# Performance work log

Hardware: AMD Instinct MI355X
Metric: run time of the kernel (lower is better)

The kernel has to match this reference:

```python
import jax, jax.numpy as jnp
import numpy as np

INPUT, HIDDEN, OUTPUT = 512, 1024, 512


def setup_inputs() -> dict:
    key = jax.random.key(0)
    k1, k2, k3, k4, k5 = jax.random.split(key, 5)
    fan = INPUT + HIDDEN
    s = 1.0 / np.sqrt(fan)
    so = 1.0 / np.sqrt(HIDDEN)
    return {
        "x": jax.random.normal(k1, (64, 512, INPUT), dtype=jnp.float32),
        "W": jax.random.uniform(k2, (fan, 4 * HIDDEN), jnp.float32, -s, s),
        "b": jax.random.uniform(k3, (4 * HIDDEN,), jnp.float32, -s, s),
        "W_out": jax.random.uniform(k4, (HIDDEN, OUTPUT), jnp.float32, -so, so),
        "b_out": jax.random.uniform(k5, (OUTPUT,), jnp.float32, -so, so),
    }


def reference(x, W, b, W_out, b_out):
    B, T, _ = x.shape
    h = HIDDEN
    h0 = jnp.zeros((B, h), dtype=x.dtype)
    c0 = jnp.zeros((B, h), dtype=x.dtype)

    def step(carry, xt):
        hs, cs = carry
        # fused gate pre-activation: [B, 4h]
        f = jnp.concatenate([xt, hs], axis=1) @ W + b
        fg = jax.nn.sigmoid(f[:, :h])          # forget gate
        ig = jax.nn.sigmoid(f[:, h:2 * h])     # input gate
        gg = jnp.tanh(f[:, 2 * h:3 * h])       # candidate
        og = jax.nn.sigmoid(f[:, 3 * h:])      # output gate
        cs = cs * fg + ig * gg
        hs = og * jnp.tanh(cs)
        return (hs, cs), None

    (hT, _), _ = jax.lax.scan(step, (h0, c0), jnp.swapaxes(x, 0, 1))
    return hT @ W_out + b_out
```

## Files before the change

### kernel.cpp

```cpp
#include <hip/hip_runtime.h>


#define B_   64
#define T_   512
#define IN_  512
#define H_   1024
#define G4_  4096
#define OUT_ 512

typedef _Float16 f16;
typedef _Float16 f16x8 __attribute__((ext_vector_type(8)));
typedef _Float16 f16x4 __attribute__((ext_vector_type(4)));
typedef float f32x4  __attribute__((ext_vector_type(4)));
typedef float f32x16 __attribute__((ext_vector_type(16)));

#define X16_OFF   0UL
#define WOT_OFF   33554432UL
#define H_OFF     (WOT_OFF + 1048576UL)
#define FLG_OFF   (H_OFF + 262144UL)
#define WS_NEED   (FLG_OFF + 8192UL)
#define ZERO_BYTES (262144UL + 8192UL)

__device__ __forceinline__ float sigmoidf_(float v) { return 1.f / (1.f + __expf(-v)); }
__device__ __forceinline__ float tanhf_(float v) { return 1.f - 2.f / (__expf(2.f * v) + 1.f); }

__device__ __forceinline__ f16x8 ld_agent_b128(const f16* p) {
  f16x8 r;
  asm volatile("global_load_dwordx4 %0, %1, off sc0 sc1" : "=v"(r) : "v"(p));
  return r;
}

__device__ __forceinline__ void st_agent_b128(f16* p, f16x8 v) {
  asm volatile("global_store_dwordx4 %0, %1, off sc0 sc1" :: "v"(p), "v"(v) : "memory");
}

__device__ __forceinline__ void wait_vm0() {
  asm volatile("s_waitcnt vmcnt(0)" ::: "memory");
  __builtin_amdgcn_sched_barrier(0);
}

__global__ __launch_bounds__(256) void lstm_prepass(
    const float* __restrict__ x, const float* __restrict__ Wout,
    f16* __restrict__ x16, f16* __restrict__ WoT) {
  long i = (long)blockIdx.x * blockDim.x + threadIdx.x;
  long stride = (long)gridDim.x * blockDim.x;
  const long n4 = (long)B_ * T_ * IN_ / 4;
  const float4* x4 = (const float4*)x;
  f16x4* o4 = (f16x4*)x16;
  for (long p = i; p < n4; p += stride) {
    float4 v = x4[p];
    f16x4 o = { (f16)v.x, (f16)v.y, (f16)v.z, (f16)v.w };
    o4[p] = o;
  }
  const long nw = (long)H_ * OUT_;
  for (long p = i; p < nw; p += stride) {
    long k = p / OUT_, c = p % OUT_;
    WoT[c * (long)H_ + k] = (f16)Wout[p];
  }
}

__global__ __launch_bounds__(512, 2) void lstm_main(
    const float* __restrict__ W, const float* __restrict__ b,
    const f16* __restrict__ x16, f16* hbuf, unsigned int* flags) {

  const int wg   = blockIdx.x;
  const int g    = wg >> 6;
  const int wgi  = wg & 63;
  const int tid  = threadIdx.x;
  const int wave = tid >> 6;
  const int lane = tid & 63;

  const int hbase   = wgi * 16;
  const int colLane = lane & 31;
  const int khalf   = (lane >> 5) * 8;
  const int arow    = lane & 31;

  f16x8 wf[24];
  #pragma unroll
  for (int n = 0; n < 2; ++n) {
    const int gate = n * 2 + (colLane >> 4);
    const int gcol = gate * H_ + hbase + (colLane & 15);
    #pragma unroll
    for (int kf = 0; kf < 12; ++kf) {
      const int k0 = (kf < 4) ? (64 * wave + 16 * kf)
                              : (512 + 128 * wave + 16 * (kf - 4));
      f16x8 v;
      #pragma unroll
      for (int j = 0; j < 8; ++j)
        v[j] = (f16)W[(long)(k0 + khalf + j) * G4_ + gcol];
      wf[n * 12 + kf] = v;
    }
  }

  const int erow = tid >> 4;
  const int ej   = tid & 15;
  float bias[4];
  #pragma unroll
  for (int gt = 0; gt < 4; ++gt) bias[gt] = b[gt * H_ + hbase + ej];

  float c_state = 0.f;

  __shared__ float red[8][32][68];
  __shared__ f16 hshare[32][16];

  const f16* xg   = x16 + (long)(g * 32) * T_ * IN_;
  f16* hb         = hbuf + (long)g * 2 * 32 * H_;
  unsigned int* flg = flags + g * 64 * 16;

  f32x16 acc0 = {}, acc1 = {};
  {
    const f16* xrow = xg + (long)arow * (T_ * IN_) + 64 * wave + khalf;
    f16x8 xa[4];
    #pragma unroll
    for (int f = 0; f < 4; ++f) xa[f] = *(const f16x8*)(xrow + 16 * f);
    #pragma unroll
    for (int kf = 0; kf < 4; ++kf) {
      acc0 = __builtin_amdgcn_mfma_f32_32x32x16_f16(xa[kf], wf[kf],      acc0, 0, 0, 0);
      acc1 = __builtin_amdgcn_mfma_f32_32x32x16_f16(xa[kf], wf[12 + kf], acc1, 0, 0, 0);
    }
  }

  for (int t = 0; t < T_; ++t) {
    if (t > 0) {
      const unsigned int tgt = (unsigned int)t;
      const unsigned int* fp = &flg[(8 * wave + (lane & 7)) << 4];
      long guard = 0;
      for (;;) {
        unsigned int v = __hip_atomic_load(fp, __ATOMIC_RELAXED,
                                           __HIP_MEMORY_SCOPE_AGENT);
        if (__all(v >= tgt) || ++guard > (1L << 22)) break;
      }
    }

    {
      const f16* hrow = hb + (long)(t & 1) * (32 * H_) + (long)arow * H_
                           + 128 * wave + khalf;
      f16x8 ha[8];
      #pragma unroll
      for (int f = 0; f < 8; ++f)
        ha[f] = ld_agent_b128(hrow + 16 * f);
      wait_vm0();
      #pragma unroll
      for (int kf = 0; kf < 8; ++kf) {
        acc0 = __builtin_amdgcn_mfma_f32_32x32x16_f16(ha[kf], wf[4 + kf],  acc0, 0, 0, 0);
        acc1 = __builtin_amdgcn_mfma_f32_32x32x16_f16(ha[kf], wf[16 + kf], acc1, 0, 0, 0);
      }
    }

    #pragma unroll
    for (int r = 0; r < 16; ++r) {
      const int row = (r & 3) + 8 * (r >> 2) + 4 * (lane >> 5);
      red[wave][row][colLane]      = acc0[r];
      red[wave][row][32 + colLane] = acc1[r];
    }
    __syncthreads();

    float f4[4];
    #pragma unroll
    for (int gt = 0; gt < 4; ++gt) {
      float s = bias[gt];
      #pragma unroll
      for (int w = 0; w < 8; ++w) s += red[w][erow][gt * 16 + ej];
      f4[gt] = s;
    }
    const float fg = sigmoidf_(f4[0]);
    const float ig = sigmoidf_(f4[1]);
    const float gg = tanhf_(f4[2]);
    const float og = sigmoidf_(f4[3]);
    c_state = c_state * fg + ig * gg;
    hshare[erow][ej] = (f16)(og * tanhf_(c_state));
    __syncthreads();

    if (wave == 0) {
      const int row = lane >> 1, half = lane & 1;
      f16x8 hv = *(const f16x8*)&hshare[row][half * 8];
      st_agent_b128(&hb[(long)((t + 1) & 1) * (32 * H_) + (long)row * H_
                        + hbase + half * 8], hv);
      wait_vm0();
      if (lane == 0)
        __hip_atomic_store(&flg[wgi << 4], (unsigned int)(t + 1),
                           __ATOMIC_RELAXED, __HIP_MEMORY_SCOPE_AGENT);
    }

    acc0 = f32x16{}; acc1 = f32x16{};
    if (t + 1 < T_) {
      const f16* xrow = xg + (long)arow * (T_ * IN_) + (long)(t + 1) * IN_
                           + 64 * wave + khalf;
      f16x8 xa[4];
      #pragma unroll
      for (int f = 0; f < 4; ++f) xa[f] = *(const f16x8*)(xrow + 16 * f);
      #pragma unroll
      for (int kf = 0; kf < 4; ++kf) {
        acc0 = __builtin_amdgcn_mfma_f32_32x32x16_f16(xa[kf], wf[kf],      acc0, 0, 0, 0);
        acc1 = __builtin_amdgcn_mfma_f32_32x32x16_f16(xa[kf], wf[12 + kf], acc1, 0, 0, 0);
      }
    }
  }
}

__global__ __launch_bounds__(256) void lstm_out(
    const f16* __restrict__ hbuf, const f16* __restrict__ WoT,
    const float* __restrict__ bout, float* __restrict__ out) {
  const int wgid = blockIdx.x;
  const int rowT = wgid >> 5;
  const int colT = wgid & 31;
  const int tid  = threadIdx.x;
  const int wave = tid >> 6;
  const int lane = tid & 63;
  const int r16  = lane & 15;
  const int ksel = (lane >> 4) * 8;

  const int g = rowT >> 1;
  const f16* hrow = hbuf + (long)g * 2 * 32 * H_
                  + (long)((rowT & 1) * 16 + r16) * H_;
  const f16* wrow = WoT + (long)(colT * 16 + r16) * H_;

  f32x4 acc = {};
  #pragma unroll
  for (int f = 0; f < 8; ++f) {
    f16x8 a  = *(const f16x8*)(hrow + 256 * wave + 32 * f + ksel);
    f16x8 bf = *(const f16x8*)(wrow + 256 * wave + 32 * f + ksel);
    acc = __builtin_amdgcn_mfma_f32_16x16x32_f16(a, bf, acc, 0, 0, 0);
  }

  __shared__ float red[4][16][20];
  #pragma unroll
  for (int r = 0; r < 4; ++r)
    red[wave][(lane >> 4) * 4 + r][lane & 15] = acc[r];
  __syncthreads();

  const int row = tid >> 4;
  const int col = tid & 15;
  float s = bout[colT * 16 + col];
  #pragma unroll
  for (int w = 0; w < 4; ++w) s += red[w][row][col];
  out[(long)(rowT * 16 + row) * OUT_ + colT * 16 + col] = s;
}

extern "C" void kernel_launch(void* const* d_in, const int* in_sizes, int n_in,
                              void* d_out, int out_size, void* d_ws, size_t ws_size,
                              hipStream_t stream) {
  const float* x    = (const float*)d_in[0];
  const float* W    = (const float*)d_in[1];
  const float* b    = (const float*)d_in[2];
  const float* Wout = (const float*)d_in[3];
  const float* bout = (const float*)d_in[4];
  float* out = (float*)d_out;

  if (ws_size < WS_NEED) return;

  char* wsb = (char*)d_ws;
  f16* x16  = (f16*)(wsb + X16_OFF);
  f16* WoT  = (f16*)(wsb + WOT_OFF);
  f16* hbuf = (f16*)(wsb + H_OFF);
  unsigned int* flags = (unsigned int*)(wsb + FLG_OFF);

  hipMemsetAsync(wsb + H_OFF, 0, ZERO_BYTES, stream);

  lstm_prepass<<<1024, 256, 0, stream>>>(x, Wout, x16, WoT);

  lstm_main<<<128, 512, 0, stream>>>(W, b, x16, hbuf, flags);

  lstm_out<<<128, 256, 0, stream>>>(hbuf, WoT, bout, out);
}
```

Measured before the change: 2.450 ms.

## Replace per-step flags with step tags encoded in the hidden-state values

Removes the separate flag array. Each hidden value is stored in fp32 as the step tag (t mod 4) plus 0.4*h. Readers poll the h buffer directly until every 8-value chunk is within 0.5 of the expected tag, then decode it to fp16. This drops the store → wait → flag-store → flag-poll → load chain, the LDS staging of h and one __syncthreads per step; the reduction buffer is also double-buffered. In exchange the h traffic doubles, since it is fp32 with per-thread scalar stores, and correctness relies on |h| < 1 and on each 16-byte load being observed as a unit.

```diff
diff --git a/kernel.cpp b/kernel.cpp
--- a/kernel.cpp
+++ b/kernel.cpp
@@ -17,25 +17,30 @@
 #define X16_OFF   0UL
 #define WOT_OFF   33554432UL
 #define H_OFF     (WOT_OFF + 1048576UL)
-#define FLG_OFF   (H_OFF + 262144UL)
-#define WS_NEED   (FLG_OFF + 8192UL)
-#define ZERO_BYTES (262144UL + 8192UL)
+#define WS_NEED   (H_OFF + 524288UL)
+#define ZERO_BYTES 524288UL
+
+#define ENCK 0.4f
+#define DECK 2.5f
 
 __device__ __forceinline__ float sigmoidf_(float v) { return 1.f / (1.f + __expf(-v)); }
 __device__ __forceinline__ float tanhf_(float v) { return 1.f - 2.f / (__expf(2.f * v) + 1.f); }
 
-__device__ __forceinline__ f16x8 ld_agent_b128(const f16* p) {
-  f16x8 r;
+__device__ __forceinline__ f32x4 ld_agent_f32x4(const float* p) {
+  f32x4 r;
   asm volatile("global_load_dwordx4 %0, %1, off sc0 sc1" : "=v"(r) : "v"(p));
   return r;
 }
-
-__device__ __forceinline__ void st_agent_b128(f16* p, f16x8 v) {
-  asm volatile("global_store_dwordx4 %0, %1, off sc0 sc1" :: "v"(p), "v"(v) : "memory");
+__device__ __forceinline__ void st_agent_f32(float* p, float v) {
+  asm volatile("global_store_dword %0, %1, off sc0 sc1" :: "v"(p), "v"(v) : "memory");
 }
 
 __device__ __forceinline__ void wait_vm0() {
   asm volatile("s_waitcnt vmcnt(0)" ::: "memory");
+  __builtin_amdgcn_sched_barrier(0);
+}
+__device__ __forceinline__ void wait_vm1() {
+  asm volatile("s_waitcnt vmcnt(1)" ::: "memory");
   __builtin_amdgcn_sched_barrier(0);
 }
 
@@ -61,7 +66,7 @@
 
 __global__ __launch_bounds__(512, 2) void lstm_main(
     const float* __restrict__ W, const float* __restrict__ b,
-    const f16* __restrict__ x16, f16* hbuf, unsigned int* flags) {
+    const f16* __restrict__ x16, float* hbuf) {
 
   const int wg   = blockIdx.x;
   const int g    = wg >> 6;
@@ -100,12 +105,10 @@
 
   float c_state = 0.f;
 
-  __shared__ float red[8][32][68];
-  __shared__ f16 hshare[32][16];
-
-  const f16* xg   = x16 + (long)(g * 32) * T_ * IN_;
-  f16* hb         = hbuf + (long)g * 2 * 32 * H_;
-  unsigned int* flg = flags + g * 64 * 16;
+  __shared__ float red[2][8][32][68];
+
+  const f16* xg = x16 + (long)(g * 32) * T_ * IN_;
+  float* hb     = hbuf + (long)g * 2 * 32 * H_;
 
   f32x16 acc0 = {}, acc1 = {};
   {
@@ -121,74 +124,95 @@
   }
 
   for (int t = 0; t < T_; ++t) {
-    if (t > 0) {
-      const unsigned int tgt = (unsigned int)t;
-      const unsigned int* fp = &flg[(8 * wave + (lane & 7)) << 4];
-      long guard = 0;
-      for (;;) {
-        unsigned int v = __hip_atomic_load(fp, __ATOMIC_RELAXED,
-                                           __HIP_MEMORY_SCOPE_AGENT);
-        if (__all(v >= tgt) || ++guard > (1L << 22)) break;
-      }
-    }
-
+    f16x8 ha[8];
     {
-      const f16* hrow = hb + (long)(t & 1) * (32 * H_) + (long)arow * H_
+      const float kf32 = (float)(t & 3);
+      const float* hp = hb + (long)(t & 1) * (32 * H_) + (long)arow * H_
                            + 128 * wave + khalf;
-      f16x8 ha[8];
-      #pragma unroll
-      for (int f = 0; f < 8; ++f)
-        ha[f] = ld_agent_b128(hrow + 16 * f);
-      wait_vm0();
-      #pragma unroll
-      for (int kf = 0; kf < 8; ++kf) {
-        acc0 = __builtin_amdgcn_mfma_f32_32x32x16_f16(ha[kf], wf[4 + kf],  acc0, 0, 0, 0);
-        acc1 = __builtin_amdgcn_mfma_f32_32x32x16_f16(ha[kf], wf[16 + kf], acc1, 0, 0, 0);
-      }
-    }
-
-    #pragma unroll
-    for (int r = 0; r < 16; ++r) {
-      const int row = (r & 3) + 8 * (r >> 2) + 4 * (lane >> 5);
-      red[wave][row][colLane]      = acc0[r];
-      red[wave][row][32 + colLane] = acc1[r];
-    }
-    __syncthreads();
-
-    float f4[4];
-    #pragma unroll
-    for (int gt = 0; gt < 4; ++gt) {
-      float s = bias[gt];
-      #pragma unroll
-      for (int w = 0; w < 8; ++w) s += red[w][erow][gt * 16 + ej];
-      f4[gt] = s;
-    }
-    const float fg = sigmoidf_(f4[0]);
-    const float ig = sigmoidf_(f4[1]);
-    const float gg = tanhf_(f4[2]);
-    const float og = sigmoidf_(f4[3]);
-    c_state = c_state * fg + ig * gg;
-    hshare[erow][ej] = (f16)(og * tanhf_(c_state));
-    __syncthreads();
-
-    if (wave == 0) {
-      const int row = lane >> 1, half = lane & 1;
-      f16x8 hv = *(const f16x8*)&hshare[row][half * 8];
-      st_agent_b128(&hb[(long)((t + 1) & 1) * (32 * H_) + (long)row * H_
-                        + hbase + half * 8], hv);
-      wait_vm0();
-      if (lane == 0)
-        __hip_atomic_store(&flg[wgi << 4], (unsigned int)(t + 1),
-                           __ATOMIC_RELAXED, __HIP_MEMORY_SCOPE_AGENT);
-    }
-
-    acc0 = f32x16{}; acc1 = f32x16{};
+      f32x4 hs0[8], hs1[8];
+      unsigned pend = 0xFFu;
+      int guard = 0;
+      while (pend && ++guard < (1 << 22)) {
+        #pragma unroll
+        for (int kf = 0; kf < 8; ++kf)
+          if (pend & (1u << kf)) {
+            hs0[kf] = ld_agent_f32x4(hp + 16 * kf);
+            hs1[kf] = ld_agent_f32x4(hp + 16 * kf + 4);
+          }
+        wait_vm0();
+        #pragma unroll
+        for (int kf = 0; kf < 8; ++kf)
+          if (pend & (1u << kf)) {
+            float d0 = hs0[kf][0] - kf32, d1 = hs0[kf][1] - kf32;
+            float d2 = hs0[kf][2] - kf32, d3 = hs0[kf][3] - kf32;
+            float d4 = hs1[kf][0] - kf32, d5 = hs1[kf][1] - kf32;
+            float d6 = hs1[kf][2] - kf32, d7 = hs1[kf][3] - kf32;
+            float m = fmaxf(fmaxf(fmaxf(fabsf(d0), fabsf(d1)),
+                                  fmaxf(fabsf(d2), fabsf(d3))),
+                            fmaxf(fmaxf(fabsf(d4), fabsf(d5)),
+                                  fmaxf(fabsf(d6), fabsf(d7))));
+            if (!__any(m > 0.5f)) {
+              f16x8 v;
+              v[0] = (f16)(d0 * DECK); v[1] = (f16)(d1 * DECK);
+              v[2] = (f16)(d2 * DECK); v[3] = (f16)(d3 * DECK);
+              v[4] = (f16)(d4 * DECK); v[5] = (f16)(d5 * DECK);
+              v[6] = (f16)(d6 * DECK); v[7] = (f16)(d7 * DECK);
+              ha[kf] = v;
+              pend &= ~(1u << kf);
+            }
+          }
+      }
+    }
+
+    f16x8 xa[4];
     if (t + 1 < T_) {
       const f16* xrow = xg + (long)arow * (T_ * IN_) + (long)(t + 1) * IN_
                            + 64 * wave + khalf;
-      f16x8 xa[4];
       #pragma unroll
       for (int f = 0; f < 4; ++f) xa[f] = *(const f16x8*)(xrow + 16 * f);
+    }
+
+    #pragma unroll
+    for (int kf = 0; kf < 8; ++kf) {
+      acc0 = __builtin_amdgcn_mfma_f32_32x32x16_f16(ha[kf], wf[4 + kf],  acc0, 0, 0, 0);
+      acc1 = __builtin_amdgcn_mfma_f32_32x32x16_f16(ha[kf], wf[16 + kf], acc1, 0, 0, 0);
+    }
+
+    {
+      float (*rb)[32][68] = red[t & 1];
+      #pragma unroll
+      for (int r = 0; r < 16; ++r) {
+        const int row = (r & 3) + 8 * (r >> 2) + 4 * (lane >> 5);
+        rb[wave][row][colLane]      = acc0[r];
+        rb[wave][row][32 + colLane] = acc1[r];
+      }
+    }
+    __syncthreads();
+
+    {
+      const float (*rb)[32][68] = red[t & 1];
+      float f4[4];
+      #pragma unroll
+      for (int gt = 0; gt < 4; ++gt) {
+        float s = bias[gt];
+        #pragma unroll
+        for (int w = 0; w < 8; ++w) s += rb[w][erow][gt * 16 + ej];
+        f4[gt] = s;
+      }
+      const float fg = sigmoidf_(f4[0]);
+      const float ig = sigmoidf_(f4[1]);
+      const float gg = tanhf_(f4[2]);
+      const float og = sigmoidf_(f4[3]);
+      c_state = c_state * fg + ig * gg;
+      const float hv  = og * tanhf_(c_state);
+      const float enc = fmaf(hv, ENCK, (float)((t + 1) & 3));
+      st_agent_f32(&hb[(long)((t + 1) & 1) * (32 * H_) + (long)erow * H_ + hbase + ej],
+                   enc);
+    }
+
+    acc0 = f32x16{}; acc1 = f32x16{};
+    if (t + 1 < T_) {
+      wait_vm1();
       #pragma unroll
       for (int kf = 0; kf < 4; ++kf) {
         acc0 = __builtin_amdgcn_mfma_f32_32x32x16_f16(xa[kf], wf[kf],      acc0, 0, 0, 0);
@@ -199,7 +223,7 @@
 }
 
 __global__ __launch_bounds__(256) void lstm_out(
-    const f16* __restrict__ hbuf, const f16* __restrict__ WoT,
+    const float* __restrict__ hbuf, const f16* __restrict__ WoT,
     const float* __restrict__ bout, float* __restrict__ out) {
   const int wgid = blockIdx.x;
   const int rowT = wgid >> 5;
@@ -211,14 +235,17 @@
   const int ksel = (lane >> 4) * 8;
 
   const int g = rowT >> 1;
-  const f16* hrow = hbuf + (long)g * 2 * 32 * H_
-                  + (long)((rowT & 1) * 16 + r16) * H_;
+  const float* hrow = hbuf + (long)g * 2 * 32 * H_
+                    + (long)((rowT & 1) * 16 + r16) * H_;
   const f16* wrow = WoT + (long)(colT * 16 + r16) * H_;
 
   f32x4 acc = {};
   #pragma unroll
   for (int f = 0; f < 8; ++f) {
-    f16x8 a  = *(const f16x8*)(hrow + 256 * wave + 32 * f + ksel);
+    const float* p = hrow + 256 * wave + 32 * f + ksel;
+    f16x8 a;
+    #pragma unroll
+    for (int j = 0; j < 8; ++j) a[j] = (f16)(p[j] * DECK);
     f16x8 bf = *(const f16x8*)(wrow + 256 * wave + 32 * f + ksel);
     acc = __builtin_amdgcn_mfma_f32_16x16x32_f16(a, bf, acc, 0, 0, 0);
   }
@@ -250,16 +277,15 @@
   if (ws_size < WS_NEED) return;
 
   char* wsb = (char*)d_ws;
-  f16* x16  = (f16*)(wsb + X16_OFF);
-  f16* WoT  = (f16*)(wsb + WOT_OFF);
-  f16* hbuf = (f16*)(wsb + H_OFF);
-  unsigned int* flags = (unsigned int*)(wsb + FLG_OFF);
+  f16* x16    = (f16*)(wsb + X16_OFF);
+  f16* WoT    = (f16*)(wsb + WOT_OFF);
+  float* hbuf = (float*)(wsb + H_OFF);
 
   hipMemsetAsync(wsb + H_OFF, 0, ZERO_BYTES, stream);
 
   lstm_prepass<<<1024, 256, 0, stream>>>(x, Wout, x16, WoT);
 
-  lstm_main<<<128, 512, 0, stream>>>(W, b, x16, hbuf, flags);
+  lstm_main<<<128, 512, 0, stream>>>(W, b, x16, hbuf);
 
   lstm_out<<<128, 256, 0, stream>>>(hbuf, WoT, bout, out);
 }
```

Measured after the change: 4.696 ms. 91.7% more time.

## Use per-wave flags and direct h stores to remove second block barrier

Applied to the files above, without the earlier changes.

Each wave now writes its own h values straight to global memory with 16-bit agent-scope stores and then publishes its own flag. This removes the LDS staging buffer, the second __syncthreads, and the wave-0 serialized store. Consumers poll 64 per-wave flags (one per lane) with two loads in flight, and the reduction buffer is double-buffered so the next step's writes cannot race with the current step's reads. The trade-off is more, smaller stores and more flags to poll on the cross-workgroup critical path.

```diff
diff --git a/kernel.cpp b/kernel.cpp
--- a/kernel.cpp
+++ b/kernel.cpp
@@ -18,8 +18,8 @@
 #define WOT_OFF   33554432UL
 #define H_OFF     (WOT_OFF + 1048576UL)
 #define FLG_OFF   (H_OFF + 262144UL)
-#define WS_NEED   (FLG_OFF + 8192UL)
-#define ZERO_BYTES (262144UL + 8192UL)
+#define WS_NEED   (FLG_OFF + 4096UL)
+#define ZERO_BYTES (262144UL + 4096UL)
 
 __device__ __forceinline__ float sigmoidf_(float v) { return 1.f / (1.f + __expf(-v)); }
 __device__ __forceinline__ float tanhf_(float v) { return 1.f - 2.f / (__expf(2.f * v) + 1.f); }
@@ -29,13 +29,24 @@
   asm volatile("global_load_dwordx4 %0, %1, off sc0 sc1" : "=v"(r) : "v"(p));
   return r;
 }
-
-__device__ __forceinline__ void st_agent_b128(f16* p, f16x8 v) {
-  asm volatile("global_store_dwordx4 %0, %1, off sc0 sc1" :: "v"(p), "v"(v) : "memory");
-}
-
+__device__ __forceinline__ void st_agent_b16(f16* p, f16 v) {
+  unsigned int u = (unsigned int)__builtin_bit_cast(unsigned short, v);
+  asm volatile("global_store_short %0, %1, off sc0 sc1" :: "v"(p), "v"(u) : "memory");
+}
+__device__ __forceinline__ void st_agent_b32(unsigned* p, unsigned v) {
+  asm volatile("global_store_dword %0, %1, off sc0 sc1" :: "v"(p), "v"(v) : "memory");
+}
+__device__ __forceinline__ unsigned ld_flag(const unsigned* p) {
+  unsigned r;
+  asm volatile("global_load_dword %0, %1, off sc0 sc1" : "=v"(r) : "v"(p));
+  return r;
+}
 __device__ __forceinline__ void wait_vm0() {
   asm volatile("s_waitcnt vmcnt(0)" ::: "memory");
+  __builtin_amdgcn_sched_barrier(0);
+}
+__device__ __forceinline__ void wait_vm1() {
+  asm volatile("s_waitcnt vmcnt(1)" ::: "memory");
   __builtin_amdgcn_sched_barrier(0);
 }
 
@@ -61,7 +72,7 @@
 
 __global__ __launch_bounds__(512, 2) void lstm_main(
     const float* __restrict__ W, const float* __restrict__ b,
-    const f16* __restrict__ x16, f16* hbuf, unsigned int* flags) {
+    const f16* __restrict__ x16, f16* hbuf, unsigned* flags) {
 
   const int wg   = blockIdx.x;
   const int g    = wg >> 6;
@@ -100,12 +111,14 @@
 
   float c_state = 0.f;
 
-  __shared__ float red[8][32][68];
-  __shared__ f16 hshare[32][16];
-
-  const f16* xg   = x16 + (long)(g * 32) * T_ * IN_;
-  f16* hb         = hbuf + (long)g * 2 * 32 * H_;
-  unsigned int* flg = flags + g * 64 * 16;
+  __shared__ float red[2][8][32][68];
+
+  const f16* xg = x16 + (long)(g * 32) * T_ * IN_;
+  f16* hb       = hbuf + (long)g * 2 * 32 * H_;
+  unsigned* flg = flags + g * 64 * 8;
+
+  const unsigned* fp = flg + 64 * wave + lane;
+  unsigned* myflag = flg + wgi * 8 + wave;
 
   f32x16 acc0 = {}, acc1 = {};
   {
@@ -121,19 +134,28 @@
   }
 
   for (int t = 0; t < T_; ++t) {
+    const int buf = t & 1;
+
     if (t > 0) {
-      const unsigned int tgt = (unsigned int)t;
-      const unsigned int* fp = &flg[(8 * wave + (lane & 7)) << 4];
-      long guard = 0;
+      const unsigned tgt = (unsigned)t;
+      int guard = 0;
+      unsigned v0 = ld_flag(fp);
+      unsigned v1 = 0;
       for (;;) {
-        unsigned int v = __hip_atomic_load(fp, __ATOMIC_RELAXED,
-                                           __HIP_MEMORY_SCOPE_AGENT);
-        if (__all(v >= tgt) || ++guard > (1L << 22)) break;
-      }
+        v1 = ld_flag(fp);
+        wait_vm1();
+        if (__all(v0 >= tgt) || ++guard > (1 << 22)) break;
+        v0 = ld_flag(fp);
+        wait_vm1();
+        if (__all(v1 >= tgt) || ++guard > (1 << 22)) break;
+      }
+      asm volatile("s_waitcnt vmcnt(0)" ::: "memory");
+      asm volatile("" :: "v"(v0), "v"(v1));
+      __builtin_amdgcn_sched_barrier(0);
     }
 
     {
-      const f16* hrow = hb + (long)(t & 1) * (32 * H_) + (long)arow * H_
+      const f16* hrow = hb + (long)buf * (32 * H_) + (long)arow * H_
                            + 128 * wave + khalf;
       f16x8 ha[8];
       #pragma unroll
@@ -147,39 +169,38 @@
       }
     }
 
-    #pragma unroll
-    for (int r = 0; r < 16; ++r) {
-      const int row = (r & 3) + 8 * (r >> 2) + 4 * (lane >> 5);
-      red[wave][row][colLane]      = acc0[r];
-      red[wave][row][32 + colLane] = acc1[r];
+    {
+      float (*rb)[32][68] = red[buf];
+      #pragma unroll
+      for (int r = 0; r < 16; ++r) {
+        const int row = (r & 3) + 8 * (r >> 2) + 4 * (lane >> 5);
+        rb[wave][row][colLane]      = acc0[r];
+        rb[wave][row][32 + colLane] = acc1[r];
+      }
     }
     __syncthreads();
 
-    float f4[4];
-    #pragma unroll
-    for (int gt = 0; gt < 4; ++gt) {
-      float s = bias[gt];
-      #pragma unroll
-      for (int w = 0; w < 8; ++w) s += red[w][erow][gt * 16 + ej];
-      f4[gt] = s;
-    }
-    const float fg = sigmoidf_(f4[0]);
-    const float ig = sigmoidf_(f4[1]);
-    const float gg = tanhf_(f4[2]);
-    const float og = sigmoidf_(f4[3]);
-    c_state = c_state * fg + ig * gg;
-    hshare[erow][ej] = (f16)(og * tanhf_(c_state));
-    __syncthreads();
-
-    if (wave == 0) {
-      const int row = lane >> 1, half = lane & 1;
-      f16x8 hv = *(const f16x8*)&hshare[row][half * 8];
-      st_agent_b128(&hb[(long)((t + 1) & 1) * (32 * H_) + (long)row * H_
-                        + hbase + half * 8], hv);
+    {
+      const float (*rb)[32][68] = red[buf];
+      float f4[4];
+      #pragma unroll
+      for (int gt = 0; gt < 4; ++gt) {
+        float s = bias[gt];
+        #pragma unroll
+        for (int w = 0; w < 8; ++w) s += rb[w][erow][gt * 16 + ej];
+        f4[gt] = s;
+      }
+      const float fg = sigmoidf_(f4[0]);
+      const float ig = sigmoidf_(f4[1]);
+      const float gg = tanhf_(f4[2]);
+      const float og = sigmoidf_(f4[3]);
+      c_state = c_state * fg + ig * gg;
+      const float hv = og * tanhf_(c_state);
+      st_agent_b16(&hb[(long)(buf ^ 1) * (32 * H_) + (long)erow * H_ + hbase + ej],
+                   (f16)hv);
       wait_vm0();
       if (lane == 0)
-        __hip_atomic_store(&flg[wgi << 4], (unsigned int)(t + 1),
-                           __ATOMIC_RELAXED, __HIP_MEMORY_SCOPE_AGENT);
+        st_agent_b32(myflag, (unsigned)(t + 1));
     }
 
     acc0 = f32x16{}; acc1 = f32x16{};
@@ -253,7 +274,7 @@
   f16* x16  = (f16*)(wsb + X16_OFF);
   f16* WoT  = (f16*)(wsb + WOT_OFF);
   f16* hbuf = (f16*)(wsb + H_OFF);
-  unsigned int* flags = (unsigned int*)(wsb + FLG_OFF);
+  unsigned* flags = (unsigned*)(wsb + FLG_OFF);
 
   hipMemsetAsync(wsb + H_OFF, 0, ZERO_BYTES, stream);
 
```

New measurement: 2.442 ms. About the same (-0.3%).
